# Kernel tuning notes

Hardware: AMD Instinct MI355X
Metric: run time of the kernel (lower is better)

The kernel has to match this reference:

```python
import jax, jax.numpy as jnp
import numpy as np


def silu(x):
    return x * jax.nn.sigmoid(x)


def setup_inputs() -> dict:
    key = jax.random.key(0)
    ks = jax.random.split(key, 9)
    d_model, d_inner, d_state, d_conv, dt_rank = 1024, 2048, 16, 4, 64
    B, L = 2, 1024
    s = 0.02  # weight init scale for numerical sanity
    return {
        "hidden_states": jax.random.normal(ks[0], (B, L, d_model), jnp.float32),
        "in_proj_w": jax.random.normal(ks[1], (2 * d_inner, d_model), jnp.float32) * s,
        "conv_w": jax.random.normal(ks[2], (d_inner, 1, d_conv), jnp.float32) * 0.2,
        "conv_b": jax.random.normal(ks[3], (d_inner,), jnp.float32) * 0.1,
        "x_proj_w": jax.random.normal(ks[4], (dt_rank + 2 * d_state, d_inner), jnp.float32) * s,
        "dt_proj_w": jax.random.normal(ks[5], (d_inner, dt_rank), jnp.float32) * (dt_rank ** -0.5),
        "dt_proj_b": jax.random.normal(ks[6], (d_inner,), jnp.float32) - 4.0,  # small dt like real init
        "A_log": jnp.log(jnp.tile(jnp.arange(1.0, d_state + 1.0, dtype=jnp.float32)[None, :], (d_inner, 1))),
        "D": jnp.ones((d_inner,), jnp.float32),
        "out_proj_w": jax.random.normal(ks[7], (d_model, d_inner), jnp.float32) * s,
    }


def reference(hidden_states, in_proj_w, conv_w, conv_b, x_proj_w,
              dt_proj_w, dt_proj_b, A_log, D, out_proj_w):
    Bsz, L, _ = hidden_states.shape
    d_inner, d_state = A_log.shape
    dt_rank = dt_proj_w.shape[1]
    K = conv_w.shape[-1]

    xz = jnp.einsum('bld,ed->ble', hidden_states, in_proj_w)  # (B,L,2*di)
    x, z = xz[..., :d_inner], xz[..., d_inner:]

    # causal depthwise conv1d (torch pads K-1 both sides then trims to L)
    xp = jnp.pad(x, ((0, 0), (K - 1, 0), (0, 0)))  # left-pad (B, L+K-1, di)
    w = conv_w[:, 0, :]  # (di, K)
    x = sum(xp[:, k:k + L, :] * w[:, k] for k in range(K)) + conv_b
    x = silu(x)

    x_dbl = jnp.einsum('bld,ed->ble', x, x_proj_w)  # (B,L,dt_rank+2n)
    dt = x_dbl[..., :dt_rank]
    Bm = x_dbl[..., dt_rank:dt_rank + d_state]
    Cm = x_dbl[..., dt_rank + d_state:]
    dt = jax.nn.softplus(jnp.einsum('blr,dr->bld', dt, dt_proj_w) + dt_proj_b)

    A = -jnp.exp(A_log)  # (di, n)
    deltaA = jnp.exp(jnp.einsum('bld,dn->bldn', dt, A))        # (B,L,di,n)
    deltaB_u = jnp.einsum('bld,bln,bld->bldn', dt, Bm, x)      # (B,L,di,n)

    def step(h, inp):
        dA_t, dBu_t, c_t = inp                # (B,di,n),(B,di,n),(B,n)
        h = dA_t * h + dBu_t
        y_t = jnp.einsum('bdn,bn->bd', h, c_t)
        return h, y_t

    h0 = jnp.zeros((Bsz, d_inner, d_state), deltaA.dtype)
    _, ys = jax.lax.scan(step, h0, (deltaA.transpose(1, 0, 2, 3),
                                    deltaB_u.transpose(1, 0, 2, 3),
                                    Cm.transpose(1, 0, 2)))
    y = ys.transpose(1, 0, 2) + x * D        # (B,L,di)
    y = y * silu(z)
    return jnp.einsum('bld,ed->ble', y, out_proj_w)
```

## Files before the change

kernel.cpp:

```cpp
#include <hip/hip_runtime.h>

typedef unsigned short u16;
typedef unsigned int   u32;
typedef __attribute__((ext_vector_type(8))) short bf16x8;
typedef __attribute__((ext_vector_type(4))) float f32x4;

__device__ inline float bf2f(u16 u) { return __uint_as_float(((u32)u) << 16); }
__device__ inline u16 f2bf(float f) {
  u32 u = __float_as_uint(f);
  return (u16)((u + 0x7FFFu + ((u >> 16) & 1u)) >> 16);
}

__device__ inline void gld_lds16(const u16* g, u16* l) {
  __builtin_amdgcn_global_load_lds((const __attribute__((address_space(1))) void*)g,
                                   (__attribute__((address_space(3))) void*)l,
                                   16, 0, 0);
}

__global__ __launch_bounds__(256) void cvt_k(
    const float* __restrict__ hs, const float* __restrict__ w_in,
    const float* __restrict__ w_x, const float* __restrict__ w_dt,
    const float* __restrict__ w_out,
    u16* __restrict__ hs_b, u16* __restrict__ w_in_b, u16* __restrict__ w_x_b,
    u16* __restrict__ w_dt_b, u16* __restrict__ w_out_b)
{
  u32 v = blockIdx.x * 256 + threadIdx.x;
  const float* s; u16* d; u32 loc;
  if      (v < 524288u)  { s = hs;    d = hs_b;    loc = v; }
  else if (v < 1572864u) { s = w_in;  d = w_in_b;  loc = v - 524288u; }
  else if (v < 1622016u) { s = w_x;   d = w_x_b;   loc = v - 1572864u; }
  else if (v < 1654784u) { s = w_dt;  d = w_dt_b;  loc = v - 1622016u; }
  else                   { s = w_out; d = w_out_b; loc = v - 1654784u; }
  float4 f = ((const float4*)s)[loc];
  ushort4 o;
  o.x = f2bf(f.x); o.y = f2bf(f.y); o.z = f2bf(f.z); o.w = f2bf(f.w);
  ((ushort4*)d)[loc] = o;
}

template <int EPI>
__global__ __launch_bounds__(256) void gemm_bt(
    const u16* __restrict__ A, int lda,
    const u16* __restrict__ B, int ldb,
    void* __restrict__ C, int ldc,
    int M, int N, int Klen,
    const float* __restrict__ bias)
{
  __shared__ u16 sA[128 * 32];
  __shared__ u16 sB[128 * 32];
  const int tid  = threadIdx.x;
  const int wave = tid >> 6, lane = tid & 63;
  const int row0 = blockIdx.x * 128, col0 = blockIdx.y * 128;
  const int kbase = blockIdx.z * Klen;
  const int r  = lane >> 2, c8 = (lane & 3) * 8;
  const int wm = (wave >> 1) * 64, wn = (wave & 1) * 64;
  const int tm = lane & 15, quad = lane >> 4;

  f32x4 acc[4][4];
#pragma unroll
  for (int i = 0; i < 4; ++i)
#pragma unroll
    for (int j = 0; j < 4; ++j) acc[i][j] = f32x4{0.f, 0.f, 0.f, 0.f};

  for (int k0 = kbase; k0 < kbase + Klen; k0 += 32) {
    for (int s = wave; s < 8; s += 4) {
      const u16* ga = A + (size_t)(row0 + s * 16 + r) * lda + (k0 + c8);
      gld_lds16(ga, &sA[s * 512 + lane * 8]);
      int br = col0 + s * 16 + r; br = br < N ? br : N - 1;
      const u16* gb = B + (size_t)br * ldb + (k0 + c8);
      gld_lds16(gb, &sB[s * 512 + lane * 8]);
    }
    __syncthreads();
    bf16x8 af[4], bfv[4];
#pragma unroll
    for (int i = 0; i < 4; ++i) af[i]  = *(const bf16x8*)&sA[(wm + i * 16 + tm) * 32 + quad * 8];
#pragma unroll
    for (int j = 0; j < 4; ++j) bfv[j] = *(const bf16x8*)&sB[(wn + j * 16 + tm) * 32 + quad * 8];
#pragma unroll
    for (int i = 0; i < 4; ++i)
#pragma unroll
      for (int j = 0; j < 4; ++j)
        acc[i][j] = __builtin_amdgcn_mfma_f32_16x16x32_bf16(af[i], bfv[j], acc[i][j], 0, 0, 0);
    __syncthreads();
  }

  const size_t zoff = (size_t)blockIdx.z * M * ldc;
#pragma unroll
  for (int j = 0; j < 4; ++j) {
    int col = col0 + wn + j * 16 + tm;
    if (col >= N) continue;
#pragma unroll
    for (int i = 0; i < 4; ++i) {
      int rb = row0 + wm + i * 16 + quad * 4;
      f32x4 v = acc[i][j];
#pragma unroll
      for (int t = 0; t < 4; ++t) {
        float f = v[t];
        size_t idx = (size_t)(rb + t) * ldc + col;
        if (EPI == 1) {
          f += bias[col];
          f = (f > 20.f) ? f : log1pf(__expf(f));
          ((float*)C)[idx] = f;
        } else if (EPI == 2) {
          ((float*)C)[idx] = f;
        } else if (EPI == 3) {
          ((float*)C)[zoff + idx] = f;
        } else {
          ((u16*)C)[idx] = f2bf(f);
        }
      }
    }
  }
}

template <int OUTBF>
__global__ __launch_bounds__(256) void red_k(
    const float* __restrict__ part, void* __restrict__ out, int total, int KS)
{
  int i = blockIdx.x * 256 + threadIdx.x;
  f32x4 a = ((const f32x4*)part)[i];
  for (int ks = 1; ks < KS; ++ks)
    a += ((const f32x4*)(part + (size_t)ks * total))[i];
  if (OUTBF) {
    ushort4 o; o.x = f2bf(a[0]); o.y = f2bf(a[1]); o.z = f2bf(a[2]); o.w = f2bf(a[3]);
    ((ushort4*)out)[i] = o;
  } else {
    ((f32x4*)out)[i] = a;
  }
}

__global__ __launch_bounds__(256) void conv_silu_k(
    const u16* __restrict__ xz, const float* __restrict__ cw,
    const float* __restrict__ cb, u16* __restrict__ xc)
{
  int gid = blockIdx.x * 256 + threadIdx.x;
  int d = gid & 2047;
  int row = gid >> 11;
  int l = row & 1023;
  float acc = cb[d];
#pragma unroll
  for (int k = 0; k < 4; ++k) {
    int ll = l - 3 + k;
    if (ll >= 0)
      acc += bf2f(xz[(size_t)(row - 3 + k) * 4096 + d]) * cw[d * 4 + k];
  }
  float s = acc / (1.f + __expf(-acc));
  xc[(size_t)row * 2048 + d] = f2bf(s);
}

#define SSEG 32
#define TSEG 32

__global__ __launch_bounds__(256) void scan1_k(
    const float* __restrict__ dtf,
    const u16* __restrict__ xdbl,
    const u16* __restrict__ xc,
    const float* __restrict__ A_log,
    float* __restrict__ hseg,
    float* __restrict__ sdt_o)
{
  const int L = 1024, DI = 2048;
  int d = blockIdx.x * 256 + threadIdx.x;
  int b = blockIdx.y, s = blockIdx.z;
  float cA[16], h[16];
#pragma unroll
  for (int n = 0; n < 16; ++n) { cA[n] = -__expf(A_log[d * 16 + n]); h[n] = 0.f; }
  float sdt = 0.f;
  size_t row = (size_t)b * L + s * TSEG;
  const float* pdt = dtf + row * DI + d;
  const u16*   px  = xc  + row * DI + d;
  const u16*   pB  = xdbl + row * 96 + 64;
  for (int t = 0; t < TSEG; ++t) {
    float dt = *pdt;
    float xv = bf2f(*px);
    bf16x8 Bv0 = *(const bf16x8*)(pB);
    bf16x8 Bv1 = *(const bf16x8*)(pB + 8);
    float dBu = dt * xv;
    sdt += dt;
#pragma unroll
    for (int n = 0; n < 16; ++n) {
      float dA = __expf(dt * cA[n]);
      float Bn = bf2f((u16)(n < 8 ? Bv0[n] : Bv1[n - 8]));
      h[n] = fmaf(dA, h[n], dBu * Bn);
    }
    pdt += DI; px += DI; pB += 96;
  }
  size_t o = (((size_t)s * 2 + b) * 2048 + d) * 16;
#pragma unroll
  for (int n = 0; n < 16; ++n) hseg[o + n] = h[n];
  sdt_o[((size_t)s * 2 + b) * 2048 + d] = sdt;
}

__global__ __launch_bounds__(256) void combine_k(
    float* hseg, const float* __restrict__ sdt,
    const float* __restrict__ A_log)
{
  int gid = blockIdx.x * 256 + threadIdx.x;
  int b = gid >> 15, d = (gid >> 4) & 2047, n = gid & 15;
  float cA = -__expf(A_log[d * 16 + n]);
  float carry = 0.f;
  for (int s = 0; s < SSEG; ++s) {
    size_t o = (size_t)s * 65536 + gid;
    float he = hseg[o];
    float P = __expf(cA * sdt[(size_t)s * 4096 + b * 2048 + d]);
    hseg[o] = carry;
    carry = fmaf(P, carry, he);
  }
}

__global__ __launch_bounds__(256) void scan3_k(
    const float* __restrict__ dtf,
    const u16* __restrict__ xdbl,
    u16* xcy,
    const u16* __restrict__ xz,
    const float* __restrict__ A_log,
    const float* __restrict__ Dw,
    const float* __restrict__ hstart)
{
  const int L = 1024, DI = 2048;
  int d = blockIdx.x * 256 + threadIdx.x;
  int b = blockIdx.y, s = blockIdx.z;
  float cA[16], h[16];
  size_t ho = (((size_t)s * 2 + b) * 2048 + d) * 16;
#pragma unroll
  for (int n = 0; n < 16; ++n) { cA[n] = -__expf(A_log[d * 16 + n]); h[n] = hstart[ho + n]; }
  float Dd = Dw[d];
  size_t row = (size_t)b * L + s * TSEG;
  const float* pdt = dtf + row * DI + d;
  u16*         px  = xcy + row * DI + d;
  const u16*   pz  = xz  + row * 4096 + 2048 + d;
  const u16*   pBC = xdbl + row * 96 + 64;
  for (int t = 0; t < TSEG; ++t) {
    float dt = *pdt;
    float xv = bf2f(*px);
    float zv = bf2f(*pz);
    bf16x8 Bv0 = *(const bf16x8*)(pBC);
    bf16x8 Bv1 = *(const bf16x8*)(pBC + 8);
    bf16x8 Cv0 = *(const bf16x8*)(pBC + 16);
    bf16x8 Cv1 = *(const bf16x8*)(pBC + 24);
    float dBu = dt * xv;
    float y = xv * Dd;
#pragma unroll
    for (int n = 0; n < 16; ++n) {
      float dA = __expf(dt * cA[n]);
      float Bn = bf2f((u16)(n < 8 ? Bv0[n] : Bv1[n - 8]));
      float Cn = bf2f((u16)(n < 8 ? Cv0[n] : Cv1[n - 8]));
      h[n] = fmaf(dA, h[n], dBu * Bn);
      y = fmaf(h[n], Cn, y);
    }
    float sig = 1.f / (1.f + __expf(-zv));
    *px = f2bf(y * (zv * sig));
    pdt += DI; px += DI; pz += 4096; pBC += 96;
  }
}

extern "C" void kernel_launch(void* const* d_in, const int* in_sizes, int n_in,
                              void* d_out, int out_size, void* d_ws, size_t ws_size,
                              hipStream_t stream)
{
  const float* hs    = (const float*)d_in[0];
  const float* w_in  = (const float*)d_in[1];
  const float* cw    = (const float*)d_in[2];
  const float* cb    = (const float*)d_in[3];
  const float* w_x   = (const float*)d_in[4];
  const float* w_dt  = (const float*)d_in[5];
  const float* b_dt  = (const float*)d_in[6];
  const float* A_log = (const float*)d_in[7];
  const float* Dw    = (const float*)d_in[8];
  const float* w_out = (const float*)d_in[9];

  char* p = (char*)d_ws;
  char* regionA = p;        p += (size_t)12 * 1024 * 1024;
  u16*   w_x_b  = (u16*)p;  p += (size_t)196608 * 2;
  u16*   w_dt_b = (u16*)p;  p += (size_t)131072 * 2;
  u16*   w_out_b= (u16*)p;  p += (size_t)2097152 * 2;
  u16*   xz     = (u16*)p;  p += (size_t)2048 * 4096 * 2;
  u16*   xc     = (u16*)p;  p += (size_t)2048 * 2048 * 2;
  u16*   xdbl   = (u16*)p;  p += (size_t)2048 * 96 * 2;
  float* dtf    = (float*)p;p += (size_t)2048 * 2048 * 4;
  float* pout   = (float*)p;p += (size_t)4 * 2048 * 1024 * 4;
  float* px     = (float*)p;

  u16*   hs_b   = (u16*)regionA;
  u16*   w_in_b = (u16*)(regionA + (size_t)2097152 * 2);
  float* hseg   = (float*)regionA;
  float* sdt    = (float*)(regionA + (size_t)SSEG * 65536 * 4);
  float* out    = (float*)d_out;

  cvt_k<<<8512, 256, 0, stream>>>(hs, w_in, w_x, w_dt, w_out,
                                  hs_b, w_in_b, w_x_b, w_dt_b, w_out_b);
  gemm_bt<0><<<dim3(16, 32, 1), 256, 0, stream>>>(hs_b, 1024, w_in_b, 1024, xz, 4096, 2048, 4096, 1024, nullptr);
  conv_silu_k<<<16384, 256, 0, stream>>>(xz, cw, cb, xc);
  gemm_bt<3><<<dim3(16, 1, 16), 256, 0, stream>>>(xc, 2048, w_x_b, 2048, px, 96, 2048, 96, 128, nullptr);
  red_k<1><<<192, 256, 0, stream>>>(px, xdbl, 196608, 16);
  gemm_bt<1><<<dim3(16, 16, 1), 256, 0, stream>>>(xdbl, 96, w_dt_b, 64, dtf, 2048, 2048, 2048, 64, b_dt);
  scan1_k<<<dim3(8, 2, SSEG), 256, 0, stream>>>(dtf, xdbl, xc, A_log, hseg, sdt);
  combine_k<<<256, 256, 0, stream>>>(hseg, sdt, A_log);
  scan3_k<<<dim3(8, 2, SSEG), 256, 0, stream>>>(dtf, xdbl, xc, xz, A_log, Dw, hseg);
  gemm_bt<3><<<dim3(16, 8, 4), 256, 0, stream>>>(xc, 2048, w_out_b, 2048, pout, 1024, 2048, 1024, 512, nullptr);
  red_k<0><<<2048, 256, 0, stream>>>(pout, out, 2097152, 4);
}
```

Measured before the change: 259.6 us.

## Fuse conv+x_proj into row kernel and merge three-pass scan into one kernel

```diff
diff --git a/kernel.cpp b/kernel.cpp
--- a/kernel.cpp
+++ b/kernel.cpp
@@ -100,8 +100,6 @@
           f += bias[col];
           f = (f > 20.f) ? f : log1pf(__expf(f));
           ((float*)C)[idx] = f;
-        } else if (EPI == 2) {
-          ((float*)C)[idx] = f;
         } else if (EPI == 3) {
           ((float*)C)[zoff + idx] = f;
         } else {
@@ -112,144 +110,154 @@
   }
 }
 
-template <int OUTBF>
 __global__ __launch_bounds__(256) void red_k(
-    const float* __restrict__ part, void* __restrict__ out, int total, int KS)
+    const float* __restrict__ part, float* __restrict__ out, int total, int KS)
 {
   int i = blockIdx.x * 256 + threadIdx.x;
   f32x4 a = ((const f32x4*)part)[i];
   for (int ks = 1; ks < KS; ++ks)
     a += ((const f32x4*)(part + (size_t)ks * total))[i];
-  if (OUTBF) {
-    ushort4 o; o.x = f2bf(a[0]); o.y = f2bf(a[1]); o.z = f2bf(a[2]); o.w = f2bf(a[3]);
-    ((ushort4*)out)[i] = o;
-  } else {
-    ((f32x4*)out)[i] = a;
-  }
-}
-
-__global__ __launch_bounds__(256) void conv_silu_k(
-    const u16* __restrict__ xz, const float* __restrict__ cw,
-    const float* __restrict__ cb, u16* __restrict__ xc)
-{
-  int gid = blockIdx.x * 256 + threadIdx.x;
-  int d = gid & 2047;
-  int row = gid >> 11;
-  int l = row & 1023;
-  float acc = cb[d];
-#pragma unroll
-  for (int k = 0; k < 4; ++k) {
-    int ll = l - 3 + k;
-    if (ll >= 0)
-      acc += bf2f(xz[(size_t)(row - 3 + k) * 4096 + d]) * cw[d * 4 + k];
-  }
-  float s = acc / (1.f + __expf(-acc));
-  xc[(size_t)row * 2048 + d] = f2bf(s);
-}
-
-#define SSEG 32
-#define TSEG 32
-
-__global__ __launch_bounds__(256) void scan1_k(
-    const float* __restrict__ dtf,
-    const u16* __restrict__ xdbl,
-    const u16* __restrict__ xc,
-    const float* __restrict__ A_log,
-    float* __restrict__ hseg,
-    float* __restrict__ sdt_o)
-{
-  const int L = 1024, DI = 2048;
-  int d = blockIdx.x * 256 + threadIdx.x;
-  int b = blockIdx.y, s = blockIdx.z;
-  float cA[16], h[16];
-#pragma unroll
-  for (int n = 0; n < 16; ++n) { cA[n] = -__expf(A_log[d * 16 + n]); h[n] = 0.f; }
-  float sdt = 0.f;
-  size_t row = (size_t)b * L + s * TSEG;
-  const float* pdt = dtf + row * DI + d;
-  const u16*   px  = xc  + row * DI + d;
-  const u16*   pB  = xdbl + row * 96 + 64;
-  for (int t = 0; t < TSEG; ++t) {
-    float dt = *pdt;
-    float xv = bf2f(*px);
-    bf16x8 Bv0 = *(const bf16x8*)(pB);
-    bf16x8 Bv1 = *(const bf16x8*)(pB + 8);
-    float dBu = dt * xv;
-    sdt += dt;
-#pragma unroll
-    for (int n = 0; n < 16; ++n) {
-      float dA = __expf(dt * cA[n]);
-      float Bn = bf2f((u16)(n < 8 ? Bv0[n] : Bv1[n - 8]));
-      h[n] = fmaf(dA, h[n], dBu * Bn);
-    }
-    pdt += DI; px += DI; pB += 96;
-  }
-  size_t o = (((size_t)s * 2 + b) * 2048 + d) * 16;
-#pragma unroll
-  for (int n = 0; n < 16; ++n) hseg[o + n] = h[n];
-  sdt_o[((size_t)s * 2 + b) * 2048 + d] = sdt;
-}
-
-__global__ __launch_bounds__(256) void combine_k(
-    float* hseg, const float* __restrict__ sdt,
-    const float* __restrict__ A_log)
-{
-  int gid = blockIdx.x * 256 + threadIdx.x;
-  int b = gid >> 15, d = (gid >> 4) & 2047, n = gid & 15;
-  float cA = -__expf(A_log[d * 16 + n]);
-  float carry = 0.f;
-  for (int s = 0; s < SSEG; ++s) {
-    size_t o = (size_t)s * 65536 + gid;
-    float he = hseg[o];
-    float P = __expf(cA * sdt[(size_t)s * 4096 + b * 2048 + d]);
-    hseg[o] = carry;
-    carry = fmaf(P, carry, he);
-  }
-}
-
-__global__ __launch_bounds__(256) void scan3_k(
+  ((f32x4*)out)[i] = a;
+}
+
+__global__ __launch_bounds__(256) void row_fuse_k(
+    const u16* __restrict__ xz,
+    const float* __restrict__ cw,
+    const float* __restrict__ cb,
+    const u16* __restrict__ w_x_b,
+    u16* __restrict__ xc,
+    u16* __restrict__ xdbl)
+{
+  __shared__ u16   xrow[8][2048];
+  __shared__ u16   we[4][2048];
+  __shared__ float xdl[8][96];
+  const int tid = threadIdx.x;
+  const int r0 = blockIdx.x * 8;
+
+  for (int i = tid; i < 8 * 2048; i += 256) {
+    int ri = i >> 11, d = i & 2047;
+    int r = r0 + ri, l = r & 1023;
+    float acc = cb[d];
+#pragma unroll
+    for (int k = 0; k < 4; ++k) {
+      int ll = l - 3 + k;
+      if (ll >= 0) acc += bf2f(xz[(size_t)(r - 3 + k) * 4096 + d]) * cw[d * 4 + k];
+    }
+    float s = acc / (1.f + __expf(-acc));
+    u16 sb = f2bf(s);
+    xrow[ri][d] = sb;
+    xc[(size_t)r * 2048 + d] = sb;
+  }
+  __syncthreads();
+
+  const int wave = tid >> 6, lane = tid & 63;
+  const int ra = wave * 2, rb2 = wave * 2 + 1;
+  for (int ec = 0; ec < 96; ec += 4) {
+    for (int i = tid; i < 4 * 2048; i += 256)
+      we[i >> 11][i & 2047] = w_x_b[(size_t)(ec + (i >> 11)) * 2048 + (i & 2047)];
+    __syncthreads();
+#pragma unroll
+    for (int e4 = 0; e4 < 4; ++e4) {
+      float p0 = 0.f, p1 = 0.f;
+      for (int k8 = lane; k8 < 256; k8 += 64) {
+        bf16x8 wv = *(const bf16x8*)&we[e4][k8 * 8];
+        bf16x8 a0 = *(const bf16x8*)&xrow[ra][k8 * 8];
+        bf16x8 a1 = *(const bf16x8*)&xrow[rb2][k8 * 8];
+#pragma unroll
+        for (int q = 0; q < 8; ++q) {
+          float wq = bf2f((u16)wv[q]);
+          p0 = fmaf(bf2f((u16)a0[q]), wq, p0);
+          p1 = fmaf(bf2f((u16)a1[q]), wq, p1);
+        }
+      }
+#pragma unroll
+      for (int s = 32; s; s >>= 1) { p0 += __shfl_xor(p0, s, 64); p1 += __shfl_xor(p1, s, 64); }
+      if (lane == 0) { xdl[ra][ec + e4] = p0; xdl[rb2][ec + e4] = p1; }
+    }
+    __syncthreads();
+  }
+
+  for (int i = tid; i < 8 * 96; i += 256) {
+    int ri = i / 96, e = i - ri * 96;
+    xdbl[(size_t)(r0 + ri) * 96 + e] = f2bf(xdl[ri][e]);
+  }
+}
+
+__global__ __launch_bounds__(256) void scan_fused_k(
     const float* __restrict__ dtf,
     const u16* __restrict__ xdbl,
     u16* xcy,
     const u16* __restrict__ xz,
     const float* __restrict__ A_log,
-    const float* __restrict__ Dw,
-    const float* __restrict__ hstart)
-{
-  const int L = 1024, DI = 2048;
-  int d = blockIdx.x * 256 + threadIdx.x;
-  int b = blockIdx.y, s = blockIdx.z;
-  float cA[16], h[16];
-  size_t ho = (((size_t)s * 2 + b) * 2048 + d) * 16;
-#pragma unroll
-  for (int n = 0; n < 16; ++n) { cA[n] = -__expf(A_log[d * 16 + n]); h[n] = hstart[ho + n]; }
+    const float* __restrict__ Dw)
+{
+  __shared__ float sm[2 * 8 * 545];
+  float* hend = sm;
+  float* Pl   = sm + 8 * 545;
+  const int tid = threadIdx.x;
+  const int ch = tid & 7, seg = tid >> 3;
+  const int d = blockIdx.x * 8 + ch;
+  const int b = blockIdx.y;
+  float cA[16];
+#pragma unroll
+  for (int n = 0; n < 16; ++n) cA[n] = -__expf(A_log[d * 16 + n]);
+  const size_t rbase = (size_t)b * 1024 + seg * 32;
+
+  float h[16];
+#pragma unroll
+  for (int n = 0; n < 16; ++n) h[n] = 0.f;
+  float sdt = 0.f;
+  for (int t = 0; t < 32; ++t) {
+    size_t row = rbase + t;
+    float dt = dtf[row * 2048 + d];
+    float xv = bf2f(xcy[row * 2048 + d]);
+    bf16x8 Bv0 = *(const bf16x8*)(xdbl + row * 96 + 64);
+    bf16x8 Bv1 = *(const bf16x8*)(xdbl + row * 96 + 72);
+    float dBu = dt * xv;
+    sdt += dt;
+#pragma unroll
+    for (int n = 0; n < 16; ++n) {
+      float Bn = bf2f((u16)(n < 8 ? Bv0[n] : Bv1[n - 8]));
+      h[n] = fmaf(__expf(dt * cA[n]), h[n], dBu * Bn);
+    }
+  }
+  const int base = ch * 545 + seg * 17;
+#pragma unroll
+  for (int n = 0; n < 16; ++n) { hend[base + n] = h[n]; Pl[base + n] = __expf(cA[n] * sdt); }
+  __syncthreads();
+
+  float c[16];
+#pragma unroll
+  for (int n = 0; n < 16; ++n) c[n] = 0.f;
+  for (int j = 0; j < seg; ++j) {
+    const int bj = ch * 545 + j * 17;
+#pragma unroll
+    for (int n = 0; n < 16; ++n) c[n] = fmaf(Pl[bj + n], c[n], hend[bj + n]);
+  }
+
   float Dd = Dw[d];
-  size_t row = (size_t)b * L + s * TSEG;
-  const float* pdt = dtf + row * DI + d;
-  u16*         px  = xcy + row * DI + d;
-  const u16*   pz  = xz  + row * 4096 + 2048 + d;
-  const u16*   pBC = xdbl + row * 96 + 64;
-  for (int t = 0; t < TSEG; ++t) {
-    float dt = *pdt;
-    float xv = bf2f(*px);
-    float zv = bf2f(*pz);
-    bf16x8 Bv0 = *(const bf16x8*)(pBC);
-    bf16x8 Bv1 = *(const bf16x8*)(pBC + 8);
-    bf16x8 Cv0 = *(const bf16x8*)(pBC + 16);
-    bf16x8 Cv1 = *(const bf16x8*)(pBC + 24);
+#pragma unroll
+  for (int n = 0; n < 16; ++n) h[n] = c[n];
+  for (int t = 0; t < 32; ++t) {
+    size_t row = rbase + t;
+    float dt = dtf[row * 2048 + d];
+    float xv = bf2f(xcy[row * 2048 + d]);
+    float zv = bf2f(xz[row * 4096 + 2048 + d]);
+    bf16x8 Bv0 = *(const bf16x8*)(xdbl + row * 96 + 64);
+    bf16x8 Bv1 = *(const bf16x8*)(xdbl + row * 96 + 72);
+    bf16x8 Cv0 = *(const bf16x8*)(xdbl + row * 96 + 80);
+    bf16x8 Cv1 = *(const bf16x8*)(xdbl + row * 96 + 88);
     float dBu = dt * xv;
     float y = xv * Dd;
 #pragma unroll
     for (int n = 0; n < 16; ++n) {
-      float dA = __expf(dt * cA[n]);
       float Bn = bf2f((u16)(n < 8 ? Bv0[n] : Bv1[n - 8]));
       float Cn = bf2f((u16)(n < 8 ? Cv0[n] : Cv1[n - 8]));
-      h[n] = fmaf(dA, h[n], dBu * Bn);
+      h[n] = fmaf(__expf(dt * cA[n]), h[n], dBu * Bn);
       y = fmaf(h[n], Cn, y);
     }
     float sig = 1.f / (1.f + __expf(-zv));
-    *px = f2bf(y * (zv * sig));
-    pdt += DI; px += DI; pz += 4096; pBC += 96;
+    xcy[row * 2048 + d] = f2bf(y * (zv * sig));
   }
 }
 
@@ -269,7 +277,8 @@
   const float* w_out = (const float*)d_in[9];
 
   char* p = (char*)d_ws;
-  char* regionA = p;        p += (size_t)12 * 1024 * 1024;
+  u16*   hs_b   = (u16*)p;  p += (size_t)2097152 * 2;
+  u16*   w_in_b = (u16*)p;  p += (size_t)4194304 * 2;
   u16*   w_x_b  = (u16*)p;  p += (size_t)196608 * 2;
   u16*   w_dt_b = (u16*)p;  p += (size_t)131072 * 2;
   u16*   w_out_b= (u16*)p;  p += (size_t)2097152 * 2;
@@ -277,25 +286,15 @@
   u16*   xc     = (u16*)p;  p += (size_t)2048 * 2048 * 2;
   u16*   xdbl   = (u16*)p;  p += (size_t)2048 * 96 * 2;
   float* dtf    = (float*)p;p += (size_t)2048 * 2048 * 4;
-  float* pout   = (float*)p;p += (size_t)4 * 2048 * 1024 * 4;
-  float* px     = (float*)p;
-
-  u16*   hs_b   = (u16*)regionA;
-  u16*   w_in_b = (u16*)(regionA + (size_t)2097152 * 2);
-  float* hseg   = (float*)regionA;
-  float* sdt    = (float*)(regionA + (size_t)SSEG * 65536 * 4);
+  float* pout   = (float*)p;
   float* out    = (float*)d_out;
 
   cvt_k<<<8512, 256, 0, stream>>>(hs, w_in, w_x, w_dt, w_out,
                                   hs_b, w_in_b, w_x_b, w_dt_b, w_out_b);
   gemm_bt<0><<<dim3(16, 32, 1), 256, 0, stream>>>(hs_b, 1024, w_in_b, 1024, xz, 4096, 2048, 4096, 1024, nullptr);
-  conv_silu_k<<<16384, 256, 0, stream>>>(xz, cw, cb, xc);
-  gemm_bt<3><<<dim3(16, 1, 16), 256, 0, stream>>>(xc, 2048, w_x_b, 2048, px, 96, 2048, 96, 128, nullptr);
-  red_k<1><<<192, 256, 0, stream>>>(px, xdbl, 196608, 16);
+  row_fuse_k<<<256, 256, 0, stream>>>(xz, cw, cb, w_x_b, xc, xdbl);
   gemm_bt<1><<<dim3(16, 16, 1), 256, 0, stream>>>(xdbl, 96, w_dt_b, 64, dtf, 2048, 2048, 2048, 64, b_dt);
-  scan1_k<<<dim3(8, 2, SSEG), 256, 0, stream>>>(dtf, xdbl, xc, A_log, hseg, sdt);
-  combine_k<<<256, 256, 0, stream>>>(hseg, sdt, A_log);
-  scan3_k<<<dim3(8, 2, SSEG), 256, 0, stream>>>(dtf, xdbl, xc, xz, A_log, Dw, hseg);
+  scan_fused_k<<<dim3(256, 2), 256, 0, stream>>>(dtf, xdbl, xc, xz, A_log, Dw);
   gemm_bt<3><<<dim3(16, 8, 4), 256, 0, stream>>>(xc, 2048, w_out_b, 2048, pout, 1024, 2048, 1024, 512, nullptr);
-  red_k<0><<<2048, 256, 0, stream>>>(pout, out, 2097152, 4);
-}
+  red_k<<<2048, 256, 0, stream>>>(pout, out, 2097152, 4);
+}
```

After: 398.3 us. 1.53x slower.
